# Performance work log

Measured on AMD Instinct MI355X. Metric: run time of the kernel, lower is better.

Reference implementation:

```python
import jax, jax.numpy as jnp
import numpy as np

CHUNK = 1024
HEAD_DIM = 128

def setup_inputs() -> dict:
    key = jax.random.key(0)
    k1, k2, k3 = jax.random.split(key, 3)
    B, H, S, D = 2, 16, 4096, HEAD_DIM
    q = jax.random.normal(k1, (B, H, S, D), dtype=jnp.float32)
    k = jax.random.normal(k2, (B, H, S, D), dtype=jnp.float32)
    v = jax.random.normal(k3, (B, H, S, D), dtype=jnp.float32)
    return {"q": q, "k": k, "v": v}

def reference(q, k, v):
    # Faithful to the torch module INCLUDING its masking bug: for every chunk
    # the triu mask uses diagonal=1 in chunk-local coordinates, so chunk-local
    # query row i attends only keys j<=i, i.e. only the first CHUNK keys matter.
    B, H, S, D = q.shape
    scale = D ** (-0.5)
    n = S // CHUNK
    qc = q.reshape(B, H, n, CHUNK, D)           # [B,H,n,C,D]
    kc = k[:, :, :CHUNK, :]                      # [B,H,C,D]
    vc = v[:, :, :CHUNK, :]                      # [B,H,C,D]
    scores = jnp.einsum('bhnid,bhjd->bhnij', qc, kc) * scale  # [B,H,n,C,C]
    mask = jnp.triu(jnp.ones((CHUNK, CHUNK), dtype=bool), 1)   # j > i masked
    scores = jnp.where(mask, -jnp.inf, scores)
    probs = jax.nn.softmax(scores, axis=-1)
    out = jnp.einsum('bhnij,bhjd->bhnid', probs, vc)
    return out.reshape(B, H, S, D)
```

## Files before the change

### kernel.cpp

```cpp
#include <hip/hip_runtime.h>


typedef __attribute__((ext_vector_type(8))) short bfrag_t;
typedef __attribute__((ext_vector_type(16))) float f32x16;
typedef unsigned short u16;
typedef unsigned int   u32;

#define SEQ     4096
#define SCHUNK  1024
#define HD      128
#define NTILE   16
#define TILE_E  8192

__device__ __forceinline__ u16 f2bf(float f) {
    union { float f; unsigned u; } x; x.f = f;
    unsigned r = x.u + 0x7fffu + ((x.u >> 16) & 1u);
    return (u16)(r >> 16);
}

__global__ __launch_bounds__(256)
void mea_prep(const float* __restrict__ kg, const float* __restrict__ vg,
              u16* __restrict__ wsK, u16* __restrict__ wsV)
{
    const int tid  = threadIdx.x;
    const int tile = blockIdx.x;
    const int bh = tile >> 4, kt = tile & 15;
    const long gsrc = (long)bh * SEQ * HD + (long)kt * 64 * HD;
    const long gdst = (long)tile * TILE_E;

#pragma unroll
    for (int i = 0; i < 4; ++i) {
        int oid = i * 256 + tid;
        int j = oid >> 4, s = oid & 15;
        const float* kp = kg + gsrc + j * HD + s * 8;
        float4 a = *(const float4*)kp;
        float4 b = *(const float4*)(kp + 4);
        bfrag_t f;
        f[0]=f2bf(a.x); f[1]=f2bf(a.y); f[2]=f2bf(a.z); f[3]=f2bf(a.w);
        f[4]=f2bf(b.x); f[5]=f2bf(b.y); f[6]=f2bf(b.z); f[7]=f2bf(b.w);
        *(bfrag_t*)(wsK + gdst + j * 128 + ((s ^ (j & 15)) * 8)) = f;
    }
#pragma unroll
    for (int i = 0; i < 4; ++i) {
        int oid = i * 256 + tid;
        int jo = oid >> 7, d = oid & 127;
        const float* vp = vg + gsrc + jo * 8 * HD + d;
        bfrag_t f;
#pragma unroll
        for (int jj = 0; jj < 8; ++jj) f[jj] = f2bf(vp[jj * HD]);
        int d2 = d >> 1;
        int S  = (jo + ((d & 1) << 3)) ^ (d2 & 15);
        *(bfrag_t*)(wsV + gdst + d2 * 128 + S * 8) = f;
    }
}

__device__ __forceinline__ void gll16(const u16* g, u16* l) {
    __builtin_amdgcn_global_load_lds((const __attribute__((address_space(1))) u32*)g,
                                     (__attribute__((address_space(3))) u32*)l, 16, 0, 0);
}

__device__ __forceinline__ float tsum16(const f32x16& p) {
    float a0 = (p[0] + p[1]) + (p[2] + p[3]);
    float a1 = (p[4] + p[5]) + (p[6] + p[7]);
    float a2 = (p[8] + p[9]) + (p[10] + p[11]);
    float a3 = (p[12] + p[13]) + (p[14] + p[15]);
    return (a0 + a1) + (a2 + a3);
}

__global__ __launch_bounds__(256, 3)
void mea_main(const float* __restrict__ qg, const u16* __restrict__ wsK,
              const u16* __restrict__ wsV, float* __restrict__ og)
{
    __shared__ __align__(16) u16 K_s[2][TILE_E];
    __shared__ __align__(16) u16 V_s[TILE_E];

    const int tid  = threadIdx.x;
    const int lane = tid & 63;
    const int wv   = tid >> 6;
    const int c31  = lane & 31;
    const int hi   = lane >> 5;

    const int x   = blockIdx.x & 7;
    const int idx = blockIdx.x >> 3;
    const int qt  = 31 - (idx >> 2);
    const int bh  = x * 4 + (idx & 3);

    const long rowbase = (long)bh * SEQ + (long)wv * SCHUNK + (long)qt * 32;
    const u16* Kb = wsK + (long)bh * NTILE * TILE_E;
    const u16* Vb = wsV + (long)bh * NTILE * TILE_E;

    bfrag_t qf[8];
    {
        const float qs = 0.12751723f;
        const float* qp = qg + (rowbase + c31) * HD + hi * 8;
#pragma unroll
        for (int ks = 0; ks < 8; ++ks) {
            float4 a = *(const float4*)(qp + ks * 16);
            float4 b = *(const float4*)(qp + ks * 16 + 4);
            bfrag_t f;
            f[0]=f2bf(a.x*qs); f[1]=f2bf(a.y*qs); f[2]=f2bf(a.z*qs); f[3]=f2bf(a.w*qs);
            f[4]=f2bf(b.x*qs); f[5]=f2bf(b.y*qs); f[6]=f2bf(b.z*qs); f[7]=f2bf(b.w*qs);
            qf[ks] = f;
        }
    }

    f32x16 oacc[4];
#pragma unroll
    for (int d = 0; d < 4; ++d)
#pragma unroll
        for (int i = 0; i < 16; ++i) oacc[d][i] = 0.f;

    float lsum = 0.f;
    const int nt   = (qt >> 1) + 1;
    const int par  = qt & 1;
    const int so   = wv * 2048 + lane * 8;
    const int ldsb = wv * 2048;

#pragma unroll
    for (int c = 0; c < 4; ++c)
        gll16(Kb + so + c * 512, &K_s[0][ldsb + c * 512]);

    int cur = 0;
    for (int kt = 0; kt < nt; ++kt) {
        __syncthreads();

#pragma unroll
        for (int c = 0; c < 4; ++c)
            gll16(Vb + (long)kt * TILE_E + so + c * 512, &V_s[ldsb + c * 512]);
        if (kt + 1 < nt) {
            const long tb = (long)(kt + 1) * TILE_E;
#pragma unroll
            for (int c = 0; c < 4; ++c)
                gll16(Kb + tb + so + c * 512, &K_s[cur ^ 1][ldsb + c * 512]);
        }

        const bool diag = (kt == nt - 1);
        const bool do1  = !(diag && par == 0);
        bfrag_t pfrag[4];

        {
            f32x16 s;
#pragma unroll
            for (int i = 0; i < 16; ++i) s[i] = 0.f;
            const u16* krow = &K_s[cur][c31 * 128];
#pragma unroll
            for (int ks = 0; ks < 8; ++ks) {
                int slot = (ks * 2 + hi) ^ (c31 & 15);
                bfrag_t kf = *(const bfrag_t*)(krow + slot * 8);
                s = __builtin_amdgcn_mfma_f32_32x32x16_bf16(kf, qf[ks], s, 0, 0, 0);
            }
            if (diag && par == 0) {
#pragma unroll
                for (int r = 0; r < 16; ++r) {
                    int crow = (r & 3) + 8 * (r >> 2) + 4 * hi;
                    if (crow > c31) s[r] = -1e30f;
                }
            }
#pragma unroll
            for (int r = 0; r < 16; ++r) s[r] = exp2f(s[r]);
            lsum += tsum16(s);
            u32 W[8];
#pragma unroll
            for (int t2 = 0; t2 < 8; ++t2)
                asm("v_cvt_pk_bf16_f32 %0, %1, %2"
                    : "=v"(W[t2]) : "v"(s[2 * t2]), "v"(s[2 * t2 + 1]));
#pragma unroll
            for (int u2 = 0; u2 < 2; ++u2) {
                u32 x0 = W[4 * u2 + 0], y0 = W[4 * u2 + 2];
                u32 x1 = W[4 * u2 + 1], y1 = W[4 * u2 + 3];
                asm("v_permlane32_swap_b32 %0, %1" : "+v"(x0), "+v"(y0));
                asm("v_permlane32_swap_b32 %0, %1" : "+v"(x1), "+v"(y1));
                union { u32 w[4]; bfrag_t f; } cvt;
                cvt.w[0] = x0; cvt.w[1] = x1; cvt.w[2] = y0; cvt.w[3] = y1;
                pfrag[u2] = cvt.f;
            }
        }
        if (do1) {
            f32x16 s;
#pragma unroll
            for (int i = 0; i < 16; ++i) s[i] = 0.f;
            const u16* krow = &K_s[cur][(32 + c31) * 128];
#pragma unroll
            for (int ks = 0; ks < 8; ++ks) {
                int slot = (ks * 2 + hi) ^ (c31 & 15);
                bfrag_t kf = *(const bfrag_t*)(krow + slot * 8);
                s = __builtin_amdgcn_mfma_f32_32x32x16_bf16(kf, qf[ks], s, 0, 0, 0);
            }
            if (diag) {
#pragma unroll
                for (int r = 0; r < 16; ++r) {
                    int crow = (r & 3) + 8 * (r >> 2) + 4 * hi;
                    if (crow > c31) s[r] = -1e30f;
                }
            }
#pragma unroll
            for (int r = 0; r < 16; ++r) s[r] = exp2f(s[r]);
            lsum += tsum16(s);
            u32 W[8];
#pragma unroll
            for (int t2 = 0; t2 < 8; ++t2)
                asm("v_cvt_pk_bf16_f32 %0, %1, %2"
                    : "=v"(W[t2]) : "v"(s[2 * t2]), "v"(s[2 * t2 + 1]));
#pragma unroll
            for (int u2 = 0; u2 < 2; ++u2) {
                u32 x0 = W[4 * u2 + 0], y0 = W[4 * u2 + 2];
                u32 x1 = W[4 * u2 + 1], y1 = W[4 * u2 + 3];
                asm("v_permlane32_swap_b32 %0, %1" : "+v"(x0), "+v"(y0));
                asm("v_permlane32_swap_b32 %0, %1" : "+v"(x1), "+v"(y1));
                union { u32 w[4]; bfrag_t f; } cvt;
                cvt.w[0] = x0; cvt.w[1] = x1; cvt.w[2] = y0; cvt.w[3] = y1;
                pfrag[2 + u2] = cvt.f;
            }
        }

        __syncthreads();

#pragma unroll
        for (int dg = 0; dg < 4; ++dg) {
            const int d  = dg * 32 + c31;
            const int d2 = d >> 1;
            const u16* vrow = &V_s[d2 * 128];
#pragma unroll
            for (int jsl = 0; jsl < 2; ++jsl) {
                int S = ((jsl * 2 + hi) + ((d & 1) << 3)) ^ (d2 & 15);
                bfrag_t vf = *(const bfrag_t*)(vrow + S * 8);
                oacc[dg] = __builtin_amdgcn_mfma_f32_32x32x16_bf16(vf, pfrag[jsl], oacc[dg], 0, 0, 0);
            }
        }
        if (do1) {
#pragma unroll
            for (int dg = 0; dg < 4; ++dg) {
                const int d  = dg * 32 + c31;
                const int d2 = d >> 1;
                const u16* vrow = &V_s[d2 * 128];
#pragma unroll
                for (int jsl = 2; jsl < 4; ++jsl) {
                    int S = ((jsl * 2 + hi) + ((d & 1) << 3)) ^ (d2 & 15);
                    bfrag_t vf = *(const bfrag_t*)(vrow + S * 8);
                    oacc[dg] = __builtin_amdgcn_mfma_f32_32x32x16_bf16(vf, pfrag[jsl], oacc[dg], 0, 0, 0);
                }
            }
        }

        cur ^= 1;
    }

    lsum += __shfl_xor(lsum, 32);
    float inv = 1.f / lsum;
#pragma unroll
    for (int dg = 0; dg < 4; ++dg) {
#pragma unroll
        for (int rq = 0; rq < 4; ++rq) {
            float4 v;
            v.x = oacc[dg][rq * 4 + 0] * inv;
            v.y = oacc[dg][rq * 4 + 1] * inv;
            v.z = oacc[dg][rq * 4 + 2] * inv;
            v.w = oacc[dg][rq * 4 + 3] * inv;
            *(float4*)(og + (rowbase + c31) * HD + dg * 32 + rq * 8 + hi * 4) = v;
        }
    }
}

extern "C" void kernel_launch(void* const* d_in, const int* in_sizes, int n_in,
                              void* d_out, int out_size, void* d_ws, size_t ws_size,
                              hipStream_t stream)
{
    (void)in_sizes; (void)n_in; (void)out_size; (void)ws_size;
    const float* q = (const float*)d_in[0];
    const float* k = (const float*)d_in[1];
    const float* v = (const float*)d_in[2];
    float* o = (float*)d_out;
    u16* wsK = (u16*)d_ws;
    u16* wsV = wsK + (size_t)32 * NTILE * TILE_E;
    mea_prep<<<dim3(512),  dim3(256), 0, stream>>>(k, v, wsK, wsV);
    mea_main<<<dim3(1024), dim3(256), 0, stream>>>(q, wsK, wsV, o);
}
```

Before: 77.61 us.

## Load K/V MFMA fragments directly from global memory, dropping LDS staging

The prep kernel now writes K and V in a fragment-major bf16 layout, so each lane's MFMA operand is one contiguous 16-byte chunk. The main kernel drops the LDS double buffer, the async global-to-LDS copies and both block barriers, and loads K and V fragments straight from global memory (L2/cache) into registers. This removes barrier stalls and LDS traffic. In exchange, the four waves of a block each fetch the same tile from global memory, and there is no software prefetch to hide load latency.

```diff
diff --git a/kernel.cpp b/kernel.cpp
--- a/kernel.cpp
+++ b/kernel.cpp
@@ -31,32 +31,25 @@
 #pragma unroll
     for (int i = 0; i < 4; ++i) {
         int oid = i * 256 + tid;
-        int j = oid >> 4, s = oid & 15;
+        int s = oid >> 6, j = oid & 63;
         const float* kp = kg + gsrc + j * HD + s * 8;
         float4 a = *(const float4*)kp;
         float4 b = *(const float4*)(kp + 4);
         bfrag_t f;
         f[0]=f2bf(a.x); f[1]=f2bf(a.y); f[2]=f2bf(a.z); f[3]=f2bf(a.w);
         f[4]=f2bf(b.x); f[5]=f2bf(b.y); f[6]=f2bf(b.z); f[7]=f2bf(b.w);
-        *(bfrag_t*)(wsK + gdst + j * 128 + ((s ^ (j & 15)) * 8)) = f;
+        *(bfrag_t*)(wsK + gdst + (s * 64 + j) * 8) = f;
     }
 #pragma unroll
     for (int i = 0; i < 4; ++i) {
         int oid = i * 256 + tid;
-        int jo = oid >> 7, d = oid & 127;
-        const float* vp = vg + gsrc + jo * 8 * HD + d;
+        int sv = oid >> 7, d = oid & 127;
+        const float* vp = vg + gsrc + sv * 8 * HD + d;
         bfrag_t f;
 #pragma unroll
         for (int jj = 0; jj < 8; ++jj) f[jj] = f2bf(vp[jj * HD]);
-        int d2 = d >> 1;
-        int S  = (jo + ((d & 1) << 3)) ^ (d2 & 15);
-        *(bfrag_t*)(wsV + gdst + d2 * 128 + S * 8) = f;
-    }
-}
-
-__device__ __forceinline__ void gll16(const u16* g, u16* l) {
-    __builtin_amdgcn_global_load_lds((const __attribute__((address_space(1))) u32*)g,
-                                     (__attribute__((address_space(3))) u32*)l, 16, 0, 0);
+        *(bfrag_t*)(wsV + gdst + (sv * 128 + d) * 8) = f;
+    }
 }
 
 __device__ __forceinline__ float tsum16(const f32x16& p) {
@@ -71,9 +64,6 @@
 void mea_main(const float* __restrict__ qg, const u16* __restrict__ wsK,
               const u16* __restrict__ wsV, float* __restrict__ og)
 {
-    __shared__ __align__(16) u16 K_s[2][TILE_E];
-    __shared__ __align__(16) u16 V_s[TILE_E];
-
     const int tid  = threadIdx.x;
     const int lane = tid & 63;
     const int wv   = tid >> 6;
@@ -111,44 +101,30 @@
         for (int i = 0; i < 16; ++i) oacc[d][i] = 0.f;
 
     float lsum = 0.f;
-    const int nt   = (qt >> 1) + 1;
-    const int par  = qt & 1;
-    const int so   = wv * 2048 + lane * 8;
-    const int ldsb = wv * 2048;
-
-#pragma unroll
-    for (int c = 0; c < 4; ++c)
-        gll16(Kb + so + c * 512, &K_s[0][ldsb + c * 512]);
-
-    int cur = 0;
+    const int nt  = (qt >> 1) + 1;
+    const int par = qt & 1;
+
+    const int kofs = (hi * 64 + c31) * 8;
+    const int vofs = (hi * 128 + c31) * 8;
+
     for (int kt = 0; kt < nt; ++kt) {
-        __syncthreads();
-
-#pragma unroll
-        for (int c = 0; c < 4; ++c)
-            gll16(Vb + (long)kt * TILE_E + so + c * 512, &V_s[ldsb + c * 512]);
-        if (kt + 1 < nt) {
-            const long tb = (long)(kt + 1) * TILE_E;
-#pragma unroll
-            for (int c = 0; c < 4; ++c)
-                gll16(Kb + tb + so + c * 512, &K_s[cur ^ 1][ldsb + c * 512]);
-        }
-
+        const u16* Kt = Kb + (long)kt * TILE_E;
+        const u16* Vt = Vb + (long)kt * TILE_E;
         const bool diag = (kt == nt - 1);
         const bool do1  = !(diag && par == 0);
         bfrag_t pfrag[4];
 
         {
+            bfrag_t kf[8];
+#pragma unroll
+            for (int ks = 0; ks < 8; ++ks)
+                kf[ks] = *(const bfrag_t*)(Kt + ks * 1024 + kofs);
             f32x16 s;
 #pragma unroll
             for (int i = 0; i < 16; ++i) s[i] = 0.f;
-            const u16* krow = &K_s[cur][c31 * 128];
-#pragma unroll
-            for (int ks = 0; ks < 8; ++ks) {
-                int slot = (ks * 2 + hi) ^ (c31 & 15);
-                bfrag_t kf = *(const bfrag_t*)(krow + slot * 8);
-                s = __builtin_amdgcn_mfma_f32_32x32x16_bf16(kf, qf[ks], s, 0, 0, 0);
-            }
+#pragma unroll
+            for (int ks = 0; ks < 8; ++ks)
+                s = __builtin_amdgcn_mfma_f32_32x32x16_bf16(kf[ks], qf[ks], s, 0, 0, 0);
             if (diag && par == 0) {
 #pragma unroll
                 for (int r = 0; r < 16; ++r) {
@@ -176,16 +152,16 @@
             }
         }
         if (do1) {
+            bfrag_t kf[8];
+#pragma unroll
+            for (int ks = 0; ks < 8; ++ks)
+                kf[ks] = *(const bfrag_t*)(Kt + ks * 1024 + 256 + kofs);
             f32x16 s;
 #pragma unroll
             for (int i = 0; i < 16; ++i) s[i] = 0.f;
-            const u16* krow = &K_s[cur][(32 + c31) * 128];
-#pragma unroll
-            for (int ks = 0; ks < 8; ++ks) {
-                int slot = (ks * 2 + hi) ^ (c31 & 15);
-                bfrag_t kf = *(const bfrag_t*)(krow + slot * 8);
-                s = __builtin_amdgcn_mfma_f32_32x32x16_bf16(kf, qf[ks], s, 0, 0, 0);
-            }
+#pragma unroll
+            for (int ks = 0; ks < 8; ++ks)
+                s = __builtin_amdgcn_mfma_f32_32x32x16_bf16(kf[ks], qf[ks], s, 0, 0, 0);
             if (diag) {
 #pragma unroll
                 for (int r = 0; r < 16; ++r) {
@@ -213,36 +189,20 @@
             }
         }
 
-        __syncthreads();
-
 #pragma unroll
         for (int dg = 0; dg < 4; ++dg) {
-            const int d  = dg * 32 + c31;
-            const int d2 = d >> 1;
-            const u16* vrow = &V_s[d2 * 128];
-#pragma unroll
-            for (int jsl = 0; jsl < 2; ++jsl) {
-                int S = ((jsl * 2 + hi) + ((d & 1) << 3)) ^ (d2 & 15);
-                bfrag_t vf = *(const bfrag_t*)(vrow + S * 8);
-                oacc[dg] = __builtin_amdgcn_mfma_f32_32x32x16_bf16(vf, pfrag[jsl], oacc[dg], 0, 0, 0);
-            }
-        }
-        if (do1) {
-#pragma unroll
-            for (int dg = 0; dg < 4; ++dg) {
-                const int d  = dg * 32 + c31;
-                const int d2 = d >> 1;
-                const u16* vrow = &V_s[d2 * 128];
-#pragma unroll
-                for (int jsl = 2; jsl < 4; ++jsl) {
-                    int S = ((jsl * 2 + hi) + ((d & 1) << 3)) ^ (d2 & 15);
-                    bfrag_t vf = *(const bfrag_t*)(vrow + S * 8);
-                    oacc[dg] = __builtin_amdgcn_mfma_f32_32x32x16_bf16(vf, pfrag[jsl], oacc[dg], 0, 0, 0);
-                }
-            }
-        }
-
-        cur ^= 1;
+            const u16* vbase = Vt + dg * 256 + vofs;
+            bfrag_t vf0 = *(const bfrag_t*)(vbase);
+            bfrag_t vf1 = *(const bfrag_t*)(vbase + 2048);
+            oacc[dg] = __builtin_amdgcn_mfma_f32_32x32x16_bf16(vf0, pfrag[0], oacc[dg], 0, 0, 0);
+            oacc[dg] = __builtin_amdgcn_mfma_f32_32x32x16_bf16(vf1, pfrag[1], oacc[dg], 0, 0, 0);
+            if (do1) {
+                bfrag_t vf2 = *(const bfrag_t*)(vbase + 4096);
+                bfrag_t vf3 = *(const bfrag_t*)(vbase + 6144);
+                oacc[dg] = __builtin_amdgcn_mfma_f32_32x32x16_bf16(vf2, pfrag[2], oacc[dg], 0, 0, 0);
+                oacc[dg] = __builtin_amdgcn_mfma_f32_32x32x16_bf16(vf3, pfrag[3], oacc[dg], 0, 0, 0);
+            }
+        }
     }
 
     lsum += __shfl_xor(lsum, 32);
```

Measured after the change: 109.7 us. 41.4% more time.
